# Kernel optimization log

Measured on AMD Instinct MI355X. Metric: run time of the kernel, lower is better.

Reference implementation:

```python
import jax, jax.numpy as jnp
import numpy as np

G, M_PER_GROUP, K, N = 8, 2048, 4096, 4096  # experts, tokens/expert, d_model, expert out dim


def setup_inputs() -> dict:
    key = jax.random.key(0)
    k1, k2, k3, k4 = jax.random.split(key, 4)
    T = G * M_PER_GROUP
    # int8 quantized activations [total_tokens, K] and per-expert weights [G, N, K] ('NT' layout)
    i8_left_tensor = jax.random.randint(k1, (T, K), -127, 128, dtype=jnp.int32).astype(jnp.int8)
    i8_right_tensors = jax.random.randint(k2, (G, N, K), -127, 128, dtype=jnp.int32).astype(jnp.int8)
    # per-token and per-(group, out-channel) dequant scales
    left_scales = jax.random.uniform(k3, (T,), jnp.float32, 0.001, 0.02)
    right_scales = jax.random.uniform(k4, (G, N), jnp.float32, 0.001, 0.02)
    tokens_per_group = jnp.full((G,), M_PER_GROUP, dtype=jnp.int32)
    return {
        "i8_left_tensor": i8_left_tensor,
        "i8_right_tensors": i8_right_tensors,
        "left_scales": left_scales,
        "right_scales": right_scales,
        "tokens_per_group": tokens_per_group,
    }


def reference(i8_left_tensor, i8_right_tensors, left_scales, right_scales, tokens_per_group):
    # moe_w8a8_group_gemm, 'NT': per group g, out_g = (A_g @ B_g^T) * ls_g[:, None] * rs_g[None, :] -> fp16
    g, n, k = i8_right_tensors.shape
    t = i8_left_tensor.shape[0]
    m = t // g  # equal-sized groups (tokens_per_group is constant M_PER_GROUP)
    a = i8_left_tensor.reshape(g, m, k).astype(jnp.float32)   # [G, M, K]
    b = i8_right_tensors.astype(jnp.float32)                  # [G, N, K]
    acc = jnp.einsum('gmk,gnk->gmn', a, b)                    # int8xint8 accum in f32
    ls = left_scales.reshape(g, m, 1)
    rs = right_scales[:, None, :]
    out = (acc * ls * rs).astype(jnp.float16)                 # fused dequant epilogue
    return out.reshape(t, n)
```

## Files before the change

kernel.cpp:

```cpp
#include <hip/hip_runtime.h>

#define GG 8
#define MPG 2048
#define KD 4096
#define ND 4096

using i32x4 = __attribute__((ext_vector_type(4))) int;

constexpr int BM = 128, BN = 128, BK = 64;

__device__ __forceinline__ int pack4(i32x4 v) {
  return (int)((unsigned)(v[0] & 0xff) | ((unsigned)(v[1] & 0xff) << 8) |
               ((unsigned)(v[2] & 0xff) << 16) | ((unsigned)(v[3] & 0xff) << 24));
}

__global__ void conv_kernel(const int* __restrict__ src, char* __restrict__ dst, long nelem) {
  long t = (long)blockIdx.x * blockDim.x + threadIdx.x;
  long stride = (long)gridDim.x * blockDim.x;
  for (long e = t * 16; e < nelem; e += stride * 16) {
    i32x4 x0 = *(const i32x4*)(src + e);
    i32x4 x1 = *(const i32x4*)(src + e + 4);
    i32x4 x2 = *(const i32x4*)(src + e + 8);
    i32x4 x3 = *(const i32x4*)(src + e + 12);
    i32x4 p;
    p[0] = pack4(x0); p[1] = pack4(x1); p[2] = pack4(x2); p[3] = pack4(x3);
    *(i32x4*)(dst + e) = p;
  }
}

__device__ __forceinline__ void gload_lds16(const void* g, void* l) {
  __builtin_amdgcn_global_load_lds(
      (const __attribute__((address_space(1))) unsigned int*)g,
      (__attribute__((address_space(3))) unsigned int*)l, 16, 0, 0);
}

template<bool DIRECT>
__global__ __launch_bounds__(256) void gemm_i8(
    const void* __restrict__ Aptr,
    const void* __restrict__ Bptr,
    const float* __restrict__ ls,
    const float* __restrict__ rs,
    float* __restrict__ out,
    int g0)
{
  __shared__ char lA[BM * BK];
  __shared__ char lB[BN * BK];

  const int gl = blockIdx.z;
  const int g = g0 + gl;
  const int bm = blockIdx.y * BM;
  const int bn = blockIdx.x * BN;

  const int tid = threadIdx.x;
  const int lane = tid & 63;
  const int wave = tid >> 6;
  const int wr = (wave >> 1) * 64;
  const int wc = (wave & 1) * 64;

  const int r16 = lane & 15;
  const int kb = (lane >> 4) * 16;

  i32x4 acc[4][4] = {};

  if constexpr (!DIRECT) {
    const char* Ag = (const char*)Aptr + ((size_t)gl * MPG + bm) * KD;
    const char* Bg = (const char*)Bptr + ((size_t)gl * ND + bn) * KD;
    const int srow = tid >> 2;
    const int skoff = (tid & 3) * 16;
    const char* pa0 = Ag + (size_t)srow * KD + skoff;
    const char* pa1 = Ag + (size_t)(srow + 64) * KD + skoff;
    const char* pb0 = Bg + (size_t)srow * KD + skoff;
    const char* pb1 = Bg + (size_t)(srow + 64) * KD + skoff;
    char* la0 = lA + wave * 1024;
    char* la1 = lA + 4096 + wave * 1024;
    char* lb0 = lB + wave * 1024;
    char* lb1 = lB + 4096 + wave * 1024;

    for (int k0 = 0; k0 < KD; k0 += BK) {
      gload_lds16(pa0 + k0, la0);
      gload_lds16(pa1 + k0, la1);
      gload_lds16(pb0 + k0, lb0);
      gload_lds16(pb1 + k0, lb1);
      __syncthreads();
      i32x4 af[4], bf[4];
#pragma unroll
      for (int m = 0; m < 4; ++m)
        af[m] = *(const i32x4*)(lA + (wr + m * 16 + r16) * BK + kb);
#pragma unroll
      for (int n = 0; n < 4; ++n)
        bf[n] = *(const i32x4*)(lB + (wc + n * 16 + r16) * BK + kb);
#pragma unroll
      for (int m = 0; m < 4; ++m)
#pragma unroll
        for (int n = 0; n < 4; ++n)
          acc[m][n] = __builtin_amdgcn_mfma_i32_16x16x64_i8(af[m], bf[n], acc[m][n], 0, 0, 0);
      __syncthreads();
    }
  } else {
    const int* Ag = (const int*)Aptr + ((size_t)gl * MPG + bm) * KD;
    const int* Bg = (const int*)Bptr + ((size_t)gl * ND + bn) * KD;
    const int drow = tid >> 1;
    const int dk = (tid & 1) * 32;

    for (int k0 = 0; k0 < KD; k0 += BK) {
      int pa[8], pb[8];
#pragma unroll
      for (int j = 0; j < 8; ++j)
        pa[j] = pack4(*(const i32x4*)(Ag + (size_t)drow * KD + k0 + dk + j * 4));
#pragma unroll
      for (int j = 0; j < 8; ++j)
        pb[j] = pack4(*(const i32x4*)(Bg + (size_t)drow * KD + k0 + dk + j * 4));
      __syncthreads();
      *(i32x4*)(lA + drow * 64 + dk)      = *(i32x4*)(pa);
      *(i32x4*)(lA + drow * 64 + dk + 16) = *(i32x4*)(pa + 4);
      *(i32x4*)(lB + drow * 64 + dk)      = *(i32x4*)(pb);
      *(i32x4*)(lB + drow * 64 + dk + 16) = *(i32x4*)(pb + 4);
      __syncthreads();
      i32x4 af[4], bf[4];
#pragma unroll
      for (int m = 0; m < 4; ++m)
        af[m] = *(const i32x4*)(lA + (wr + m * 16 + r16) * BK + kb);
#pragma unroll
      for (int n = 0; n < 4; ++n)
        bf[n] = *(const i32x4*)(lB + (wc + n * 16 + r16) * BK + kb);
#pragma unroll
      for (int m = 0; m < 4; ++m)
#pragma unroll
        for (int n = 0; n < 4; ++n)
          acc[m][n] = __builtin_amdgcn_mfma_i32_16x16x64_i8(af[m], bf[n], acc[m][n], 0, 0, 0);
    }
  }

  const size_t trow0 = (size_t)g * MPG + bm + wr + (lane >> 4) * 4;
  const int col0 = bn + wc + r16;
  float rsv[4];
#pragma unroll
  for (int n = 0; n < 4; ++n) rsv[n] = rs[(size_t)g * ND + col0 + n * 16];
#pragma unroll
  for (int m = 0; m < 4; ++m) {
#pragma unroll
    for (int r = 0; r < 4; ++r) {
      size_t row = trow0 + m * 16 + r;
      float lsv = ls[row];
#pragma unroll
      for (int n = 0; n < 4; ++n)
        out[row * ND + col0 + n * 16] = (float)acc[m][n][r] * lsv * rsv[n];
    }
  }
}

extern "C" void kernel_launch(void* const* d_in, const int* in_sizes, int n_in,
                              void* d_out, int out_size, void* d_ws, size_t ws_size,
                              hipStream_t stream) {
  const int* A32 = (const int*)d_in[0];
  const int* B32 = (const int*)d_in[1];
  const float* ls = (const float*)d_in[2];
  const float* rs = (const float*)d_in[3];
  float* out = (float*)d_out;

  const size_t aE = (size_t)GG * MPG * KD;
  const size_t bE = (size_t)GG * ND * KD;
  const size_t aSlab = (size_t)MPG * KD;
  const size_t bSlab = (size_t)ND * KD;

  dim3 blk(256);
  if (d_ws && ws_size >= aE + bE) {
    char* wsA = (char*)d_ws;
    char* wsB = wsA + aE;
    conv_kernel<<<8192, 256, 0, stream>>>(A32, wsA, (long)aE);
    conv_kernel<<<16384, 256, 0, stream>>>(B32, wsB, (long)bE);
    dim3 grid(ND / BN, MPG / BM, GG);
    gemm_i8<false><<<grid, blk, 0, stream>>>(wsA, wsB, ls, rs, out, 0);
  } else if (d_ws && ws_size >= aSlab + bSlab) {
    char* wsA = (char*)d_ws;
    char* wsB = wsA + aSlab;
    for (int g = 0; g < GG; ++g) {
      conv_kernel<<<2048, 256, 0, stream>>>(A32 + (size_t)g * aSlab, wsA, (long)aSlab);
      conv_kernel<<<4096, 256, 0, stream>>>(B32 + (size_t)g * bSlab, wsB, (long)bSlab);
      dim3 grid(ND / BN, MPG / BM, 1);
      gemm_i8<false><<<grid, blk, 0, stream>>>(wsA, wsB, ls, rs, out, g);
    }
  } else {
    dim3 grid(ND / BN, MPG / BM, GG);
    gemm_i8<true><<<grid, blk, 0, stream>>>(A32, B32, ls, rs, out, 0);
  }
}
```

Baseline: 563.9 us.

## Add 256x256 double-buffered int8 GEMM kernel with swizzled LDS and XCD remap

```diff
diff --git a/kernel.cpp b/kernel.cpp
--- a/kernel.cpp
+++ b/kernel.cpp
@@ -6,8 +6,6 @@
 #define ND 4096
 
 using i32x4 = __attribute__((ext_vector_type(4))) int;
-
-constexpr int BM = 128, BN = 128, BK = 64;
 
 __device__ __forceinline__ int pack4(i32x4 v) {
   return (int)((unsigned)(v[0] & 0xff) | ((unsigned)(v[1] & 0xff) << 8) |
@@ -34,14 +32,123 @@
       (__attribute__((address_space(3))) unsigned int*)l, 16, 0, 0);
 }
 
-template<bool DIRECT>
-__global__ __launch_bounds__(256) void gemm_i8(
-    const void* __restrict__ Aptr,
-    const void* __restrict__ Bptr,
+constexpr int NT = KD / 128;
+
+__global__ __launch_bounds__(512, 2) void gemm256_i8(
+    const char* __restrict__ Aall,
+    const char* __restrict__ Ball,
     const float* __restrict__ ls,
     const float* __restrict__ rs,
     float* __restrict__ out,
-    int g0)
+    int g0, int nwg)
+{
+  extern __shared__ char lds[];
+
+  const int tid  = threadIdx.x;
+  const int lane = tid & 63;
+  const int wave = tid >> 6;
+
+  int bid = blockIdx.x;
+  int wg  = (bid & 7) * (nwg >> 3) + (bid >> 3);
+  const int gl = wg >> 7;
+  const int rr_ = wg & 127;
+  const int bm = (rr_ >> 4) * 256;
+  const int bn = (rr_ & 15) * 256;
+  const int g  = g0 + gl;
+
+  const int srow = tid >> 3;
+  const int scol = ((tid & 7) << 4) ^ ((srow & 7) << 4);
+  const char* Ag = Aall + ((size_t)gl * MPG + bm) * KD;
+  const char* Bg = Ball + ((size_t)gl * ND  + bn) * KD;
+  const char* pa[4]; const char* pb[4];
+#pragma unroll
+  for (int i = 0; i < 4; ++i) {
+    pa[i] = Ag + (size_t)(i * 64 + srow) * KD + scol;
+    pb[i] = Bg + (size_t)(i * 64 + srow) * KD + scol;
+  }
+  char* wbase = lds + wave * 1024;
+
+  auto stage = [&](int buf, int kt) {
+    const int ko = kt << 7;
+    char* d = wbase + buf * 65536;
+#pragma unroll
+    for (int i = 0; i < 4; ++i) gload_lds16(pa[i] + ko, d + i * 8192);
+#pragma unroll
+    for (int i = 0; i < 4; ++i) gload_lds16(pb[i] + ko, d + 32768 + i * 8192);
+  };
+
+  const int wm = wave >> 2;
+  const int wn = wave & 3;
+  const int r16 = lane & 15;
+  const int klane = (lane >> 4) << 4;
+  const int sx = (r16 & 7) << 4;
+  const char* aBase0 = lds + (size_t)(wm * 128 + r16) * 128;
+  const char* bBase0 = lds + 32768 + (size_t)(wn * 64 + r16) * 128;
+
+  i32x4 acc[8][4] = {};
+
+  auto compute = [&](int buf) {
+    const char* pA = aBase0 + buf * 65536;
+    const char* pB = bBase0 + buf * 65536;
+#pragma unroll
+    for (int ks = 0; ks < 2; ++ks) {
+      const int kx = ((ks << 6) + klane) ^ sx;
+      i32x4 bf[4], af[8];
+#pragma unroll
+      for (int n = 0; n < 4; ++n) bf[n] = *(const i32x4*)(pB + n * 2048 + kx);
+#pragma unroll
+      for (int m = 0; m < 8; ++m) af[m] = *(const i32x4*)(pA + m * 2048 + kx);
+      __builtin_amdgcn_s_setprio(1);
+#pragma unroll
+      for (int m = 0; m < 8; ++m)
+#pragma unroll
+        for (int n = 0; n < 4; ++n)
+          acc[m][n] = __builtin_amdgcn_mfma_i32_16x16x64_i8(af[m], bf[n], acc[m][n], 0, 0, 0);
+      __builtin_amdgcn_s_setprio(0);
+    }
+  };
+
+  stage(0, 0);
+  stage(1, 1);
+#pragma unroll 1
+  for (int kt = 0; kt < NT; ++kt) {
+    const int cur = kt & 1;
+    if (kt + 1 < NT) { asm volatile("s_waitcnt vmcnt(8)" ::: "memory"); }
+    else             { asm volatile("s_waitcnt vmcnt(0)" ::: "memory"); }
+    __builtin_amdgcn_s_barrier();
+    asm volatile("" ::: "memory");
+    compute(cur);
+    asm volatile("" ::: "memory");
+    __builtin_amdgcn_s_barrier();
+    asm volatile("" ::: "memory");
+    if (kt + 2 < NT) stage(cur, kt + 2);
+  }
+
+  const size_t orow0 = (size_t)g * MPG + bm + wm * 128 + ((lane >> 4) << 2);
+  const int col0 = bn + wn * 64 + r16;
+  float rsv[4];
+#pragma unroll
+  for (int n = 0; n < 4; ++n) rsv[n] = rs[(size_t)g * ND + col0 + n * 16];
+#pragma unroll
+  for (int m = 0; m < 8; ++m) {
+#pragma unroll
+    for (int q = 0; q < 4; ++q) {
+      size_t row = orow0 + m * 16 + q;
+      float lsv = ls[row];
+#pragma unroll
+      for (int n = 0; n < 4; ++n)
+        out[row * ND + col0 + n * 16] = (float)acc[m][n][q] * lsv * rsv[n];
+    }
+  }
+}
+
+constexpr int BM = 128, BN = 128, BK = 64;
+
+template<bool DIRECT>
+__global__ __launch_bounds__(256) void gemm_i8(
+    const void* __restrict__ Aptr, const void* __restrict__ Bptr,
+    const float* __restrict__ ls, const float* __restrict__ rs,
+    float* __restrict__ out, int g0)
 {
   __shared__ char lA[BM * BK];
   __shared__ char lB[BN * BK];
@@ -50,13 +157,11 @@
   const int g = g0 + gl;
   const int bm = blockIdx.y * BM;
   const int bn = blockIdx.x * BN;
-
   const int tid = threadIdx.x;
   const int lane = tid & 63;
   const int wave = tid >> 6;
   const int wr = (wave >> 1) * 64;
   const int wc = (wave & 1) * 64;
-
   const int r16 = lane & 15;
   const int kb = (lane >> 4) * 16;
 
@@ -84,11 +189,9 @@
       __syncthreads();
       i32x4 af[4], bf[4];
 #pragma unroll
-      for (int m = 0; m < 4; ++m)
-        af[m] = *(const i32x4*)(lA + (wr + m * 16 + r16) * BK + kb);
-#pragma unroll
-      for (int n = 0; n < 4; ++n)
-        bf[n] = *(const i32x4*)(lB + (wc + n * 16 + r16) * BK + kb);
+      for (int m = 0; m < 4; ++m) af[m] = *(const i32x4*)(lA + (wr + m * 16 + r16) * BK + kb);
+#pragma unroll
+      for (int n = 0; n < 4; ++n) bf[n] = *(const i32x4*)(lB + (wc + n * 16 + r16) * BK + kb);
 #pragma unroll
       for (int m = 0; m < 4; ++m)
 #pragma unroll
@@ -105,11 +208,9 @@
     for (int k0 = 0; k0 < KD; k0 += BK) {
       int pa[8], pb[8];
 #pragma unroll
-      for (int j = 0; j < 8; ++j)
-        pa[j] = pack4(*(const i32x4*)(Ag + (size_t)drow * KD + k0 + dk + j * 4));
-#pragma unroll
-      for (int j = 0; j < 8; ++j)
-        pb[j] = pack4(*(const i32x4*)(Bg + (size_t)drow * KD + k0 + dk + j * 4));
+      for (int j = 0; j < 8; ++j) pa[j] = pack4(*(const i32x4*)(Ag + (size_t)drow * KD + k0 + dk + j * 4));
+#pragma unroll
+      for (int j = 0; j < 8; ++j) pb[j] = pack4(*(const i32x4*)(Bg + (size_t)drow * KD + k0 + dk + j * 4));
       __syncthreads();
       *(i32x4*)(lA + drow * 64 + dk)      = *(i32x4*)(pa);
       *(i32x4*)(lA + drow * 64 + dk + 16) = *(i32x4*)(pa + 4);
@@ -118,11 +219,9 @@
       __syncthreads();
       i32x4 af[4], bf[4];
 #pragma unroll
-      for (int m = 0; m < 4; ++m)
-        af[m] = *(const i32x4*)(lA + (wr + m * 16 + r16) * BK + kb);
-#pragma unroll
-      for (int n = 0; n < 4; ++n)
-        bf[n] = *(const i32x4*)(lB + (wc + n * 16 + r16) * BK + kb);
+      for (int m = 0; m < 4; ++m) af[m] = *(const i32x4*)(lA + (wr + m * 16 + r16) * BK + kb);
+#pragma unroll
+      for (int n = 0; n < 4; ++n) bf[n] = *(const i32x4*)(lB + (wc + n * 16 + r16) * BK + kb);
 #pragma unroll
       for (int m = 0; m < 4; ++m)
 #pragma unroll
@@ -139,12 +238,12 @@
 #pragma unroll
   for (int m = 0; m < 4; ++m) {
 #pragma unroll
-    for (int r = 0; r < 4; ++r) {
-      size_t row = trow0 + m * 16 + r;
+    for (int q = 0; q < 4; ++q) {
+      size_t row = trow0 + m * 16 + q;
       float lsv = ls[row];
 #pragma unroll
       for (int n = 0; n < 4; ++n)
-        out[row * ND + col0 + n * 16] = (float)acc[m][n][r] * lsv * rsv[n];
+        out[row * ND + col0 + n * 16] = (float)acc[m][n][q] * lsv * rsv[n];
     }
   }
 }
@@ -163,25 +262,38 @@
   const size_t aSlab = (size_t)MPG * KD;
   const size_t bSlab = (size_t)ND * KD;
 
-  dim3 blk(256);
+  const int smem = 131072;
+  static_assert(131072 == 2 * (32768 + 32768), "lds layout");
+  bool big_lds_ok =
+      hipFuncSetAttribute((const void*)gemm256_i8,
+                          hipFuncAttributeMaxDynamicSharedMemorySize, smem) == hipSuccess;
+
   if (d_ws && ws_size >= aE + bE) {
     char* wsA = (char*)d_ws;
     char* wsB = wsA + aE;
     conv_kernel<<<8192, 256, 0, stream>>>(A32, wsA, (long)aE);
     conv_kernel<<<16384, 256, 0, stream>>>(B32, wsB, (long)bE);
-    dim3 grid(ND / BN, MPG / BM, GG);
-    gemm_i8<false><<<grid, blk, 0, stream>>>(wsA, wsB, ls, rs, out, 0);
+    if (big_lds_ok) {
+      gemm256_i8<<<1024, 512, smem, stream>>>(wsA, wsB, ls, rs, out, 0, 1024);
+    } else {
+      dim3 grid(ND / BN, MPG / BM, GG);
+      gemm_i8<false><<<grid, dim3(256), 0, stream>>>(wsA, wsB, ls, rs, out, 0);
+    }
   } else if (d_ws && ws_size >= aSlab + bSlab) {
     char* wsA = (char*)d_ws;
     char* wsB = wsA + aSlab;
-    for (int g = 0; g < GG; ++g) {
-      conv_kernel<<<2048, 256, 0, stream>>>(A32 + (size_t)g * aSlab, wsA, (long)aSlab);
-      conv_kernel<<<4096, 256, 0, stream>>>(B32 + (size_t)g * bSlab, wsB, (long)bSlab);
-      dim3 grid(ND / BN, MPG / BM, 1);
-      gemm_i8<false><<<grid, blk, 0, stream>>>(wsA, wsB, ls, rs, out, g);
+    for (int gidx = 0; gidx < GG; ++gidx) {
+      conv_kernel<<<2048, 256, 0, stream>>>(A32 + (size_t)gidx * aSlab, wsA, (long)aSlab);
+      conv_kernel<<<4096, 256, 0, stream>>>(B32 + (size_t)gidx * bSlab, wsB, (long)bSlab);
+      if (big_lds_ok) {
+        gemm256_i8<<<128, 512, smem, stream>>>(wsA, wsB, ls, rs, out, gidx, 128);
+      } else {
+        dim3 grid(ND / BN, MPG / BM, 1);
+        gemm_i8<false><<<grid, dim3(256), 0, stream>>>(wsA, wsB, ls, rs, out, gidx);
+      }
     }
   } else {
     dim3 grid(ND / BN, MPG / BM, GG);
-    gemm_i8<true><<<grid, blk, 0, stream>>>(A32, B32, ls, rs, out, 0);
-  }
-}
+    gemm_i8<true><<<grid, dim3(256), 0, stream>>>(A32, B32, ls, rs, out, 0);
+  }
+}
```

New measurement: 499.5 us. 11.4% less time.
